# Optimization experiments

Measured on AMD Instinct MI355X. Metric: run time of the kernel, lower is better.

## Reference

```python
import jax, jax.numpy as jnp
import numpy as np

B, N, D, H = 2, 1536, 1024, 16
DH = D // H
SCALE = DH ** -0.5


def setup_inputs() -> dict:
    key = jax.random.key(0)
    ks = jax.random.split(key, 16)
    s = D ** -0.5
    x = jax.random.normal(ks[0], (B, N, D), dtype=jnp.float32)
    # causal prior: 0 on/below diagonal, -1e9 above
    causal = jnp.tril(jnp.ones((N, N), dtype=bool))
    attn_bias = jnp.where(causal, 0.0, -1e9).astype(jnp.float32)[None, None]
    mk = lambda k, shp: jax.random.normal(k, shp, dtype=jnp.float32) * s
    return {
        "x": x,
        "attn_bias": attn_bias,
        "Wq": mk(ks[1], (D, D)), "bq": jnp.zeros((D,), jnp.float32),
        "Wk": mk(ks[2], (D, D)), "bk": jnp.zeros((D,), jnp.float32),
        "Wv": mk(ks[3], (D, D)), "bv": jnp.zeros((D,), jnp.float32),
        "Wg1": mk(ks[4], (D, D)), "bg1": jnp.zeros((D,), jnp.float32),
        "Wg2": mk(ks[5], (D, 1)), "bg2": jnp.zeros((1,), jnp.float32),
        "Wo": mk(ks[6], (D, D)), "bo": jnp.zeros((D,), jnp.float32),
    }


def reference(x, attn_bias, Wq, bq, Wk, bk, Wv, bv, Wg1, bg1, Wg2, bg2, Wo, bo):
    b, n, d = x.shape
    # projections -> [B, H, N, DH]
    split = lambda t: t.reshape(b, n, H, DH).swapaxes(1, 2)
    Q = split(x @ Wq + bq)
    K = split(x @ Wk + bk)
    V = split(x @ Wv + bv)
    # scores [B, H, N, N]
    attn = jnp.einsum("bhnd,bhmd->bhnm", Q, K) * SCALE + attn_bias
    attn = jax.nn.softmax(attn, axis=-1)
    # per-(batch, head, query) entropy over key axis
    entropy = -(attn * jnp.log(attn + 1e-6)).sum(-1)  # [B, H, N]
    # gate MLP (torch nn.GELU default is exact erf)
    gate = jax.nn.sigmoid(jax.nn.gelu(x @ Wg1 + bg1, approximate=False) @ Wg2 + bg2)  # [B, N, 1]
    attn = attn * gate[:, None, :, :]  # broadcast over heads, keys
    out = jnp.einsum("bhnm,bhmd->bhnd", attn, V)
    out = out.swapaxes(1, 2).reshape(b, n, d) @ Wo + bo
    return out, entropy
```

## Files before the change

kernel.cpp:

```cpp
#include <hip/hip_runtime.h>
#include <hip/hip_bf16.h>
#include <math.h>

#define Bsz  2
#define Nseq 1536
#define Dmod 1024
#define NH   16
#define DHd  64
#define MTOT (Bsz*Nseq)
#define SCALE 0.125f
#define BK   32

typedef short  short8 __attribute__((ext_vector_type(8)));
typedef float  f32x4  __attribute__((ext_vector_type(4)));
typedef unsigned short u16x4 __attribute__((ext_vector_type(4)));
typedef unsigned short ushortT;

__device__ __forceinline__ float b2f(__hip_bfloat16 v) { return __bfloat162float(v); }
__device__ __forceinline__ unsigned short f2bf(float f) {
    union { float f; unsigned u; } a; a.f = f;
    unsigned r = a.u + 0x7fffu + ((a.u >> 16) & 1u);
    return (unsigned short)(r >> 16);
}

__device__ __forceinline__ void gl2lds16(const ushortT* g, ushortT* lds) {
    __builtin_amdgcn_global_load_lds(
        (const __attribute__((address_space(1))) unsigned int*)(g),
        (__attribute__((address_space(3))) unsigned int*)(lds),
        16, 0, 0);
}

__global__ __launch_bounds__(256)
void prep_kernel(const float* W0, const float* W1, const float* W2,
                 const float* W3, const float* W4,
                 ushortT* T0, ushortT* T1, ushortT* T2, ushortT* T3, ushortT* T4,
                 const float* __restrict__ x, ushortT* __restrict__ xb,
                 float* __restrict__ glogit)
{
    const int z = blockIdx.z;
    const int t = threadIdx.x;
    if (z == 5) {
        const int bi = blockIdx.y * 16 + blockIdx.x;
        const size_t NEl = (size_t)MTOT * Dmod;
        for (size_t i = ((size_t)bi * 256 + t) * 4; i < NEl; i += (size_t)256 * 256 * 4) {
            float4 v = *(const float4*)(x + i);
            u16x4 o = { f2bf(v.x), f2bf(v.y), f2bf(v.z), f2bf(v.w) };
            *(u16x4*)(xb + i) = o;
        }
        if (t < 12) glogit[bi * 12 + t] = 0.f;
        return;
    }
    __shared__ float tile[64][65];
    const float* W = z == 0 ? W0 : z == 1 ? W1 : z == 2 ? W2 : z == 3 ? W3 : W4;
    ushortT*     T = z == 0 ? T0 : z == 1 ? T1 : z == 2 ? T2 : z == 3 ? T3 : T4;
    const int k0 = blockIdx.x * 64, n0 = blockIdx.y * 64;
    for (int i = t; i < 1024; i += 256) {
        int r = i >> 4, c4 = (i & 15) * 4;
        float4 v = *(const float4*)&W[(size_t)(k0 + r) * 1024 + n0 + c4];
        tile[r][c4 + 0] = v.x; tile[r][c4 + 1] = v.y;
        tile[r][c4 + 2] = v.z; tile[r][c4 + 3] = v.w;
    }
    __syncthreads();
    for (int i = t; i < 1024; i += 256) {
        int rn = i >> 4, ck4 = (i & 15) * 4;
        u16x4 o = { f2bf(tile[ck4 + 0][rn]), f2bf(tile[ck4 + 1][rn]),
                    f2bf(tile[ck4 + 2][rn]), f2bf(tile[ck4 + 3][rn]) };
        *(u16x4*)&T[(size_t)(n0 + rn) * 1024 + k0 + ck4] = o;
    }
}

__device__ __forceinline__
void gemm_core(const ushortT* __restrict__ A, const ushortT* __restrict__ Bt,
               int m0, int n0, ushortT* As, ushortT* Bs, f32x4 (&acc)[4][2])
{
    const int t = threadIdx.x;
    const int l = t & 63, w = t >> 6;
    const int wm = (w >> 1) * 64, wn = (w & 1) * 32;
    const int lm = l & 15, q = l >> 4;

    const int r0 = t >> 2, c0 = (t & 3) * 8;
    const ushortT* Ag0 = A  + (size_t)(m0 + r0) * 1024 + c0;
    const ushortT* Ag1 = Ag0 + (size_t)64 * 1024;
    const ushortT* Bg0 = Bt + (size_t)(n0 + r0) * 1024 + c0;
    ushortT* La0 = As + t * 8;
    ushortT* La1 = As + 2048 + t * 8;
    ushortT* Lb0 = Bs + t * 8;

    gl2lds16(Ag0, La0);
    gl2lds16(Ag1, La1);
    gl2lds16(Bg0, Lb0);

    for (int kt = 0; kt < 1024 / BK; ++kt) {
        __syncthreads();
        if (kt + 1 < 1024 / BK) {
            int ko = (kt + 1) * BK;
            int bo = ((kt + 1) & 1) ? 4096 : 0;
            int bo2 = ((kt + 1) & 1) ? 2048 : 0;
            gl2lds16(Ag0 + ko, La0 + bo);
            gl2lds16(Ag1 + ko, La1 + bo);
            gl2lds16(Bg0 + ko, Lb0 + bo2);
        }
        const ushortT* Ab = As + ((kt & 1) ? 4096 : 0);
        const ushortT* Bb = Bs + ((kt & 1) ? 2048 : 0);
        short8 af[4], bf[2];
#pragma unroll
        for (int i = 0; i < 4; ++i)
            af[i] = *(const short8*)&Ab[(wm + i * 16 + lm) * 32 + q * 8];
#pragma unroll
        for (int j = 0; j < 2; ++j)
            bf[j] = *(const short8*)&Bb[(wn + j * 16 + lm) * 32 + q * 8];
#pragma unroll
        for (int i = 0; i < 4; ++i)
#pragma unroll
            for (int j = 0; j < 2; ++j)
                acc[i][j] = __builtin_amdgcn_mfma_f32_16x16x32_bf16(af[i], bf[j], acc[i][j], 0, 0, 0);
    }
}

__device__ __forceinline__
void gemm_core_sq(const ushortT* __restrict__ A, const ushortT* __restrict__ Bt,
                  int m0, int n0, ushortT* As, ushortT* Bs, f32x4 (&acc)[2][2])
{
    const int t = threadIdx.x;
    const int l = t & 63, w = t >> 6;
    const int wm = (w >> 1) * 32, wn = (w & 1) * 32;
    const int lm = l & 15, q = l >> 4;

    const int r0 = t >> 2, c0 = (t & 3) * 8;
    const ushortT* Ag = A  + (size_t)(m0 + r0) * 1024 + c0;
    const ushortT* Bg = Bt + (size_t)(n0 + r0) * 1024 + c0;
    ushortT* La = As + t * 8;
    ushortT* Lb = Bs + t * 8;

    gl2lds16(Ag, La);
    gl2lds16(Bg, Lb);

    for (int kt = 0; kt < 1024 / BK; ++kt) {
        __syncthreads();
        if (kt + 1 < 1024 / BK) {
            int ko = (kt + 1) * BK;
            int bo = ((kt + 1) & 1) ? 2048 : 0;
            gl2lds16(Ag + ko, La + bo);
            gl2lds16(Bg + ko, Lb + bo);
        }
        const ushortT* Ab = As + ((kt & 1) ? 2048 : 0);
        const ushortT* Bb = Bs + ((kt & 1) ? 2048 : 0);
        short8 af[2], bf[2];
#pragma unroll
        for (int i = 0; i < 2; ++i) {
            af[i] = *(const short8*)&Ab[(wm + i * 16 + lm) * 32 + q * 8];
            bf[i] = *(const short8*)&Bb[(wn + i * 16 + lm) * 32 + q * 8];
        }
#pragma unroll
        for (int i = 0; i < 2; ++i)
#pragma unroll
            for (int j = 0; j < 2; ++j)
                acc[i][j] = __builtin_amdgcn_mfma_f32_16x16x32_bf16(af[i], bf[j], acc[i][j], 0, 0, 0);
    }
}

__global__ __launch_bounds__(256)
void gemm_qkvg(const ushortT* __restrict__ xb,
               const ushortT* Wt0, const ushortT* Wt1, const ushortT* Wt2, const ushortT* Wt3,
               const float* bz0, const float* bz1, const float* bz2, const float* bz3,
               const float* __restrict__ Wg2,
               ushortT* O0, ushortT* O1, ushortT* O2, float* __restrict__ glogit)
{
    __shared__ ushortT As[2 * 128 * 32];
    __shared__ ushortT Bs[2 * 64 * 32];
    const int z = blockIdx.z;
    const ushortT* Wt  = z == 0 ? Wt0 : z == 1 ? Wt1 : z == 2 ? Wt2 : Wt3;
    const float*  bias = z == 0 ? bz0 : z == 1 ? bz1 : z == 2 ? bz2 : bz3;
    const int m0 = blockIdx.y * 128, n0 = blockIdx.x * 64;

    f32x4 acc[4][2] = {};
    gemm_core(xb, Wt, m0, n0, As, Bs, acc);

    const int t = threadIdx.x, l = t & 63, w = t >> 6;
    const int wm = (w >> 1) * 64, wn = (w & 1) * 32;
    const int lm = l & 15, q = l >> 4;

    if (z == 3) {
        float part[4][4] = {};
#pragma unroll
        for (int i = 0; i < 4; ++i)
#pragma unroll
            for (int j = 0; j < 2; ++j) {
                int n = n0 + wn + j * 16 + lm;
                float bn = bias[n];
                float w2 = Wg2[n];
#pragma unroll
                for (int r = 0; r < 4; ++r) {
                    float v = acc[i][j][r] + bn;
                    v = 0.5f * v * (1.0f + erff(v * 0.70710678118654752f));
                    part[i][r] += v * w2;
                }
            }
#pragma unroll
        for (int i = 0; i < 4; ++i)
#pragma unroll
            for (int r = 0; r < 4; ++r) {
                float p = part[i][r];
#pragma unroll
                for (int msk = 1; msk < 16; msk <<= 1) p += __shfl_xor(p, msk, 16);
                if (lm == 0)
                    atomicAdd(&glogit[m0 + wm + i * 16 + q * 4 + r], p);
            }
        return;
    }

    ushortT* O = z == 0 ? O0 : z == 1 ? O1 : O2;
#pragma unroll
    for (int i = 0; i < 4; ++i)
#pragma unroll
        for (int j = 0; j < 2; ++j) {
            int n = n0 + wn + j * 16 + lm;
            float bn = bias[n];
#pragma unroll
            for (int r = 0; r < 4; ++r) {
                int m = m0 + wm + i * 16 + q * 4 + r;
                float v = acc[i][j][r] + bn;
                if (z == 0) v *= SCALE;
                if (z == 2) {
                    int b = m / Nseq, nn = m - b * Nseq;
                    int h = n >> 6, dd = n & 63;
                    O[(size_t)((b * 16 + h) * 64 + dd) * Nseq + nn] = f2bf(v);
                } else {
                    O[(size_t)m * 1024 + n] = f2bf(v);
                }
            }
        }
}

__global__ __launch_bounds__(256)
void gemm_out(const ushortT* __restrict__ AO, const ushortT* __restrict__ WtO,
              const float* __restrict__ bias, float* __restrict__ C)
{
    __shared__ ushortT As[2 * 64 * 32];
    __shared__ ushortT Bs[2 * 64 * 32];
    const int m0 = blockIdx.y * 64, n0 = blockIdx.x * 64;

    f32x4 acc[2][2] = {};
    gemm_core_sq(AO, WtO, m0, n0, As, Bs, acc);

    const int t = threadIdx.x, l = t & 63, w = t >> 6;
    const int wm = (w >> 1) * 32, wn = (w & 1) * 32;
    const int lm = l & 15, q = l >> 4;
#pragma unroll
    for (int i = 0; i < 2; ++i)
#pragma unroll
        for (int j = 0; j < 2; ++j) {
            int n = n0 + wn + j * 16 + lm;
            float bn = bias[n];
#pragma unroll
            for (int r = 0; r < 4; ++r) {
                int m = m0 + wm + i * 16 + q * 4 + r;
                C[(size_t)m * 1024 + n] = acc[i][j][r] + bn;
            }
        }
}

__global__ __launch_bounds__(128)
void attn_mfma(const ushortT* __restrict__ Q, const ushortT* __restrict__ K,
               const ushortT* __restrict__ Vt, const float* __restrict__ glogit,
               const float* __restrict__ bg2, ushortT* __restrict__ AO,
               float* __restrict__ ent)
{
    __shared__ ushortT Ps[2][32][72];
    __shared__ float mbuf[3072];

    const int t  = threadIdx.x;
    const int w  = t >> 6, l = t & 63;
    const int ln = l & 15, q4 = l >> 4;
    const int bh = blockIdx.x, b = bh >> 4, h = bh & 15;
    const int q32 = (int)gridDim.y - 1 - (int)blockIdx.y;
    const int wq = q32 * 32;
    const int kd = wq >> 6;
    const int sbmax = ((wq >> 4) & 3) + 1;

    const ushortT* Qp = Q + (size_t)(b * Nseq + wq + ln) * Dmod + h * DHd + q4 * 8;
    short8 qf[2][2];
    qf[0][0] = *(const short8*)(Qp);
    qf[0][1] = *(const short8*)(Qp + 32);
    qf[1][0] = *(const short8*)(Qp + (size_t)16 * Dmod);
    qf[1][1] = *(const short8*)(Qp + (size_t)16 * Dmod + 32);

    float l_lane[2][4] = {}, t_lane[2][4] = {};
    f32x4 oacc[2][4] = {};

    const ushortT* Kbase = K  + (size_t)(b * Nseq) * Dmod + h * DHd + q4 * 8;
    const ushortT* Vbase = Vt + ((size_t)(b * 16 + h) * 64) * Nseq + q4 * 8;

    short8 kc[4][2];
    {
        const ushortT* Kp = Kbase + (size_t)(w * 64 + ln) * Dmod;
#pragma unroll
        for (int nb = 0; nb < 4; ++nb) {
            kc[nb][0] = *(const short8*)(Kp + (size_t)nb * 16 * Dmod);
            kc[nb][1] = *(const short8*)(Kp + (size_t)nb * 16 * Dmod + 32);
        }
    }

    for (int kt = w; kt < kd; kt += 2) {
        const int k0 = kt * 64;
        const ushortT* Vp = Vbase + (size_t)ln * Nseq + k0;
        short8 vf[4][2];
#pragma unroll
        for (int nb = 0; nb < 4; ++nb) {
            vf[nb][0] = *(const short8*)(Vp + (size_t)nb * 16 * Nseq);
            vf[nb][1] = *(const short8*)(Vp + (size_t)nb * 16 * Nseq + 32);
        }
        short8 kn[4][2];
        {
            int prow = k0 + 128; if (prow > Nseq - 64) prow = Nseq - 64;
            const ushortT* Kp = Kbase + (size_t)(prow + ln) * Dmod;
#pragma unroll
            for (int nb = 0; nb < 4; ++nb) {
                kn[nb][0] = *(const short8*)(Kp + (size_t)nb * 16 * Dmod);
                kn[nb][1] = *(const short8*)(Kp + (size_t)nb * 16 * Dmod + 32);
            }
        }
        f32x4 sacc[2][4];
#pragma unroll
        for (int g = 0; g < 2; ++g)
#pragma unroll
            for (int nb = 0; nb < 4; ++nb) {
                f32x4 a = {};
                a = __builtin_amdgcn_mfma_f32_16x16x32_bf16(qf[g][0], kc[nb][0], a, 0, 0, 0);
                a = __builtin_amdgcn_mfma_f32_16x16x32_bf16(qf[g][1], kc[nb][1], a, 0, 0, 0);
                sacc[g][nb] = a;
            }
#pragma unroll
        for (int g = 0; g < 2; ++g)
#pragma unroll
            for (int nb = 0; nb < 4; ++nb)
#pragma unroll
                for (int r = 0; r < 4; ++r) {
                    float sv = sacc[g][nb][r];
                    float ev = __expf(sv);
                    l_lane[g][r] += ev;
                    t_lane[g][r] += ev * sv;
                    Ps[w][g * 16 + q4 * 4 + r][nb * 16 + ln] = f2bf(ev);
                }
        short8 pf[2][2];
#pragma unroll
        for (int g = 0; g < 2; ++g) {
            pf[g][0] = *(const short8*)&Ps[w][g * 16 + ln][q4 * 8];
            pf[g][1] = *(const short8*)&Ps[w][g * 16 + ln][32 + q4 * 8];
        }
#pragma unroll
        for (int g = 0; g < 2; ++g)
#pragma unroll
            for (int nb = 0; nb < 4; ++nb) {
                oacc[g][nb] = __builtin_amdgcn_mfma_f32_16x16x32_bf16(pf[g][0], vf[nb][0], oacc[g][nb], 0, 0, 0);
                oacc[g][nb] = __builtin_amdgcn_mfma_f32_16x16x32_bf16(pf[g][1], vf[nb][1], oacc[g][nb], 0, 0, 0);
            }
#pragma unroll
        for (int nb = 0; nb < 4; ++nb) { kc[nb][0] = kn[nb][0]; kc[nb][1] = kn[nb][1]; }
    }

    if ((kd & 1) == w) {
        const int k0 = kd * 64;
        const ushortT* Vp = Vbase + (size_t)ln * Nseq + k0;
        short8 vf[4][2];
#pragma unroll
        for (int nb = 0; nb < 4; ++nb) {
            vf[nb][0] = *(const short8*)(Vp + (size_t)nb * 16 * Nseq);
            vf[nb][1] = *(const short8*)(Vp + (size_t)nb * 16 * Nseq + 32);
        }
        f32x4 sacc[2][4];
#pragma unroll
        for (int g = 0; g < 2; ++g)
#pragma unroll
            for (int nb = 0; nb < 4; ++nb)
                if (nb <= sbmax) {
                    f32x4 a = {};
                    a = __builtin_amdgcn_mfma_f32_16x16x32_bf16(qf[g][0], kc[nb][0], a, 0, 0, 0);
                    a = __builtin_amdgcn_mfma_f32_16x16x32_bf16(qf[g][1], kc[nb][1], a, 0, 0, 0);
                    sacc[g][nb] = a;
                }
#pragma unroll
        for (int g = 0; g < 2; ++g)
#pragma unroll
            for (int nb = 0; nb < 4; ++nb)
#pragma unroll
                for (int r = 0; r < 4; ++r) {
                    float ev = 0.f;
                    if (nb <= sbmax) {
                        int kg = k0 + nb * 16 + ln;
                        int qg = wq + g * 16 + q4 * 4 + r;
                        float sv = sacc[g][nb][r];
                        ev = (kg <= qg) ? __expf(sv) : 0.f;
                        l_lane[g][r] += ev;
                        t_lane[g][r] += ev * sv;
                    }
                    Ps[w][g * 16 + q4 * 4 + r][nb * 16 + ln] = f2bf(ev);
                }
        short8 pf[2][2];
#pragma unroll
        for (int g = 0; g < 2; ++g) {
            pf[g][0] = *(const short8*)&Ps[w][g * 16 + ln][q4 * 8];
            pf[g][1] = *(const short8*)&Ps[w][g * 16 + ln][32 + q4 * 8];
        }
#pragma unroll
        for (int g = 0; g < 2; ++g)
#pragma unroll
            for (int nb = 0; nb < 4; ++nb) {
                oacc[g][nb] = __builtin_amdgcn_mfma_f32_16x16x32_bf16(pf[g][0], vf[nb][0], oacc[g][nb], 0, 0, 0);
                oacc[g][nb] = __builtin_amdgcn_mfma_f32_16x16x32_bf16(pf[g][1], vf[nb][1], oacc[g][nb], 0, 0, 0);
            }
    }

    if (w == 1) {
#pragma unroll
        for (int g = 0; g < 2; ++g)
#pragma unroll
            for (int nb = 0; nb < 4; ++nb)
#pragma unroll
                for (int r = 0; r < 4; ++r)
                    mbuf[(((g << 2) | nb) * 4 + r) * 64 + l] = oacc[g][nb][r];
#pragma unroll
        for (int g = 0; g < 2; ++g)
#pragma unroll
            for (int r = 0; r < 4; ++r) {
                mbuf[2048 + ((g << 2) | r) * 64 + l] = l_lane[g][r];
                mbuf[2560 + ((g << 2) | r) * 64 + l] = t_lane[g][r];
            }
    }
    __syncthreads();
    if (w == 1) return;
#pragma unroll
    for (int g = 0; g < 2; ++g) {
#pragma unroll
        for (int nb = 0; nb < 4; ++nb)
#pragma unroll
            for (int r = 0; r < 4; ++r)
                oacc[g][nb][r] += mbuf[(((g << 2) | nb) * 4 + r) * 64 + l];
#pragma unroll
        for (int r = 0; r < 4; ++r) {
            l_lane[g][r] += mbuf[2048 + ((g << 2) | r) * 64 + l];
            t_lane[g][r] += mbuf[2560 + ((g << 2) | r) * 64 + l];
        }
    }

    const float bg2v = bg2[0];
#pragma unroll
    for (int g = 0; g < 2; ++g) {
        float sc[4];
#pragma unroll
        for (int r = 0; r < 4; ++r) {
            float lv = l_lane[g][r], tv = t_lane[g][r];
#pragma unroll
            for (int msk = 1; msk < 16; msk <<= 1) {
                lv += __shfl_xor(lv, msk, 16);
                tv += __shfl_xor(tv, msk, 16);
            }
            int qg = wq + g * 16 + q4 * 4 + r;
            float inv = 1.f / lv;
            if (ln == 0)
                ent[((size_t)b * NH + h) * Nseq + qg] = logf(lv) - tv * inv;
            float logit = glogit[b * Nseq + qg] + bg2v;
            sc[r] = inv / (1.f + __expf(-logit));
        }
#pragma unroll
        for (int nb = 0; nb < 4; ++nb)
#pragma unroll
            for (int r = 0; r < 4; ++r) {
                int qg = wq + g * 16 + q4 * 4 + r;
                AO[(size_t)(b * Nseq + qg) * Dmod + h * DHd + nb * 16 + ln] =
                    f2bf(oacc[g][nb][r] * sc[r]);
            }
    }
}

extern "C" void kernel_launch(void* const* d_in, const int* in_sizes, int n_in,
                              void* d_out, int out_size, void* d_ws, size_t ws_size,
                              hipStream_t stream)
{
    const float* x   = (const float*)d_in[0];
    const float* Wq  = (const float*)d_in[2];
    const float* bq  = (const float*)d_in[3];
    const float* Wk  = (const float*)d_in[4];
    const float* bk  = (const float*)d_in[5];
    const float* Wv  = (const float*)d_in[6];
    const float* bv  = (const float*)d_in[7];
    const float* Wg1 = (const float*)d_in[8];
    const float* bg1 = (const float*)d_in[9];
    const float* Wg2 = (const float*)d_in[10];
    const float* bg2 = (const float*)d_in[11];
    const float* Wo  = (const float*)d_in[12];
    const float* bo  = (const float*)d_in[13];

    const size_t NE = (size_t)MTOT * Dmod;
    ushortT* p   = (ushortT*)d_ws;
    ushortT* Qw  = p; p += NE;
    ushortT* Kw  = p; p += NE;
    ushortT* Vtw = p; p += NE;
    ushortT* AO  = p; p += NE;
    ushortT* xb  = p; p += NE;
    ushortT* WtQ = p; p += (size_t)1024 * 1024;
    ushortT* WtK = p; p += (size_t)1024 * 1024;
    ushortT* WtV = p; p += (size_t)1024 * 1024;
    ushortT* WtG = p; p += (size_t)1024 * 1024;
    ushortT* WtO = p; p += (size_t)1024 * 1024;
    float* glogit = (float*)p;

    float* out_f = (float*)d_out;
    float* ent_f = out_f + NE;

    prep_kernel<<<dim3(16, 16, 6), 256, 0, stream>>>(Wq, Wk, Wv, Wg1, Wo,
                                                     WtQ, WtK, WtV, WtG, WtO,
                                                     x, xb, glogit);
    gemm_qkvg<<<dim3(16, 24, 4), 256, 0, stream>>>(xb, WtQ, WtK, WtV, WtG,
                                                   bq, bk, bv, bg1, Wg2,
                                                   Qw, Kw, Vtw, glogit);
    attn_mfma<<<dim3(Bsz * NH, Nseq / 32), 128, 0, stream>>>(Qw, Kw, Vtw, glogit,
                                                             bg2, AO, ent_f);
    gemm_out<<<dim3(16, 48), 256, 0, stream>>>(AO, WtO, bo, out_f);
}
```

Measured before the change: 227.4 us.

## Remap block indices for XCD-aware L2 locality and merge attention query tiles

Measured after the change: 244.1 us. +7.3%, slower.

```diff
diff --git a/kernel.cpp b/kernel.cpp
--- a/kernel.cpp
+++ b/kernel.cpp
@@ -168,10 +168,16 @@
 {
     __shared__ ushortT As[2 * 128 * 32];
     __shared__ ushortT Bs[2 * 64 * 32];
-    const int z = blockIdx.z;
+
+    const int f = (int)blockIdx.x;
+    const int cx = f & 7, j = f >> 3;
+    const int z  = j / 48;
+    const int vx = (cx & 3) * 4 + (j & 3);
+    const int vy = (cx >> 2) * 12 + ((j >> 2) % 12);
+    const int m0 = vy * 128, n0 = vx * 64;
+
     const ushortT* Wt  = z == 0 ? Wt0 : z == 1 ? Wt1 : z == 2 ? Wt2 : Wt3;
     const float*  bias = z == 0 ? bz0 : z == 1 ? bz1 : z == 2 ? bz2 : bz3;
-    const int m0 = blockIdx.y * 128, n0 = blockIdx.x * 64;
 
     f32x4 acc[4][2] = {};
     gemm_core(xb, Wt, m0, n0, As, Bs, acc);
@@ -185,13 +191,13 @@
 #pragma unroll
         for (int i = 0; i < 4; ++i)
 #pragma unroll
-            for (int j = 0; j < 2; ++j) {
-                int n = n0 + wn + j * 16 + lm;
+            for (int jj = 0; jj < 2; ++jj) {
+                int n = n0 + wn + jj * 16 + lm;
                 float bn = bias[n];
                 float w2 = Wg2[n];
 #pragma unroll
                 for (int r = 0; r < 4; ++r) {
-                    float v = acc[i][j][r] + bn;
+                    float v = acc[i][jj][r] + bn;
                     v = 0.5f * v * (1.0f + erff(v * 0.70710678118654752f));
                     part[i][r] += v * w2;
                 }
@@ -213,13 +219,13 @@
 #pragma unroll
     for (int i = 0; i < 4; ++i)
 #pragma unroll
-        for (int j = 0; j < 2; ++j) {
-            int n = n0 + wn + j * 16 + lm;
+        for (int jj = 0; jj < 2; ++jj) {
+            int n = n0 + wn + jj * 16 + lm;
             float bn = bias[n];
 #pragma unroll
             for (int r = 0; r < 4; ++r) {
                 int m = m0 + wm + i * 16 + q * 4 + r;
-                float v = acc[i][j][r] + bn;
+                float v = acc[i][jj][r] + bn;
                 if (z == 0) v *= SCALE;
                 if (z == 2) {
                     int b = m / Nseq, nn = m - b * Nseq;
@@ -238,7 +244,11 @@
 {
     __shared__ ushortT As[2 * 64 * 32];
     __shared__ ushortT Bs[2 * 64 * 32];
-    const int m0 = blockIdx.y * 64, n0 = blockIdx.x * 64;
+
+    const int f = (int)blockIdx.x;
+    const int c = f & 7, j = f >> 3;
+    const int m0 = (c * 6 + (j >> 4)) * 64;
+    const int n0 = (j & 15) * 64;
 
     f32x4 acc[2][2] = {};
     gemm_core_sq(AO, WtO, m0, n0, As, Bs, acc);
@@ -249,32 +259,38 @@
 #pragma unroll
     for (int i = 0; i < 2; ++i)
 #pragma unroll
-        for (int j = 0; j < 2; ++j) {
-            int n = n0 + wn + j * 16 + lm;
+        for (int jj = 0; jj < 2; ++jj) {
+            int n = n0 + wn + jj * 16 + lm;
             float bn = bias[n];
 #pragma unroll
             for (int r = 0; r < 4; ++r) {
                 int m = m0 + wm + i * 16 + q * 4 + r;
-                C[(size_t)m * 1024 + n] = acc[i][j][r] + bn;
-            }
-        }
-}
-
-__global__ __launch_bounds__(128)
+                C[(size_t)m * 1024 + n] = acc[i][jj][r] + bn;
+            }
+        }
+}
+
+__global__ __launch_bounds__(256)
 void attn_mfma(const ushortT* __restrict__ Q, const ushortT* __restrict__ K,
                const ushortT* __restrict__ Vt, const float* __restrict__ glogit,
                const float* __restrict__ bg2, ushortT* __restrict__ AO,
                float* __restrict__ ent)
 {
-    __shared__ ushortT Ps[2][32][72];
-    __shared__ float mbuf[3072];
+    __shared__ ushortT Ps[4][32][72];
+    __shared__ float mbuf[2][3072];
 
     const int t  = threadIdx.x;
     const int w  = t >> 6, l = t & 63;
+    const int qh = w >> 1, par = w & 1;
     const int ln = l & 15, q4 = l >> 4;
-    const int bh = blockIdx.x, b = bh >> 4, h = bh & 15;
-    const int q32 = (int)gridDim.y - 1 - (int)blockIdx.y;
-    const int wq = q32 * 32;
+
+    const int f = (int)blockIdx.x;
+    const int c = f & 7, j = f >> 3;
+    const int bh = c * 4 + (j & 3);
+    const int jj = j >> 2;
+    const int q64 = (j & 1) ? (23 - jj) : jj;
+    const int b = bh >> 4, h = bh & 15;
+    const int wq = q64 * 64 + qh * 32;
     const int kd = wq >> 6;
     const int sbmax = ((wq >> 4) & 3) + 1;
 
@@ -293,7 +309,7 @@
 
     short8 kc[4][2];
     {
-        const ushortT* Kp = Kbase + (size_t)(w * 64 + ln) * Dmod;
+        const ushortT* Kp = Kbase + (size_t)(par * 64 + ln) * Dmod;
 #pragma unroll
         for (int nb = 0; nb < 4; ++nb) {
             kc[nb][0] = *(const short8*)(Kp + (size_t)nb * 16 * Dmod);
@@ -301,7 +317,7 @@
         }
     }
 
-    for (int kt = w; kt < kd; kt += 2) {
+    for (int kt = par; kt < kd; kt += 2) {
         const int k0 = kt * 64;
         const ushortT* Vp = Vbase + (size_t)ln * Nseq + k0;
         short8 vf[4][2];
@@ -359,7 +375,7 @@
         for (int nb = 0; nb < 4; ++nb) { kc[nb][0] = kn[nb][0]; kc[nb][1] = kn[nb][1]; }
     }
 
-    if ((kd & 1) == w) {
+    if ((kd & 1) == par) {
         const int k0 = kd * 64;
         const ushortT* Vp = Vbase + (size_t)ln * Nseq + k0;
         short8 vf[4][2];
@@ -411,35 +427,35 @@
             }
     }
 
-    if (w == 1) {
+    if (par == 1) {
 #pragma unroll
         for (int g = 0; g < 2; ++g)
 #pragma unroll
             for (int nb = 0; nb < 4; ++nb)
 #pragma unroll
                 for (int r = 0; r < 4; ++r)
-                    mbuf[(((g << 2) | nb) * 4 + r) * 64 + l] = oacc[g][nb][r];
+                    mbuf[qh][(((g << 2) | nb) * 4 + r) * 64 + l] = oacc[g][nb][r];
 #pragma unroll
         for (int g = 0; g < 2; ++g)
 #pragma unroll
             for (int r = 0; r < 4; ++r) {
-                mbuf[2048 + ((g << 2) | r) * 64 + l] = l_lane[g][r];
-                mbuf[2560 + ((g << 2) | r) * 64 + l] = t_lane[g][r];
+                mbuf[qh][2048 + ((g << 2) | r) * 64 + l] = l_lane[g][r];
+                mbuf[qh][2560 + ((g << 2) | r) * 64 + l] = t_lane[g][r];
             }
     }
     __syncthreads();
-    if (w == 1) return;
+    if (par == 1) return;
 #pragma unroll
     for (int g = 0; g < 2; ++g) {
 #pragma unroll
         for (int nb = 0; nb < 4; ++nb)
 #pragma unroll
             for (int r = 0; r < 4; ++r)
-                oacc[g][nb][r] += mbuf[(((g << 2) | nb) * 4 + r) * 64 + l];
+                oacc[g][nb][r] += mbuf[qh][(((g << 2) | nb) * 4 + r) * 64 + l];
 #pragma unroll
         for (int r = 0; r < 4; ++r) {
-            l_lane[g][r] += mbuf[2048 + ((g << 2) | r) * 64 + l];
-            t_lane[g][r] += mbuf[2560 + ((g << 2) | r) * 64 + l];
+            l_lane[g][r] += mbuf[qh][2048 + ((g << 2) | r) * 64 + l];
+            t_lane[g][r] += mbuf[qh][2560 + ((g << 2) | r) * 64 + l];
         }
     }
 
@@ -511,10 +527,10 @@
     prep_kernel<<<dim3(16, 16, 6), 256, 0, stream>>>(Wq, Wk, Wv, Wg1, Wo,
                                                      WtQ, WtK, WtV, WtG, WtO,
                                                      x, xb, glogit);
-    gemm_qkvg<<<dim3(16, 24, 4), 256, 0, stream>>>(xb, WtQ, WtK, WtV, WtG,
-                                                   bq, bk, bv, bg1, Wg2,
-                                                   Qw, Kw, Vtw, glogit);
-    attn_mfma<<<dim3(Bsz * NH, Nseq / 32), 128, 0, stream>>>(Qw, Kw, Vtw, glogit,
-                                                             bg2, AO, ent_f);
-    gemm_out<<<dim3(16, 48), 256, 0, stream>>>(AO, WtO, bo, out_f);
-}
+    gemm_qkvg<<<dim3(1536), 256, 0, stream>>>(xb, WtQ, WtK, WtV, WtG,
+                                              bq, bk, bv, bg1, Wg2,
+                                              Qw, Kw, Vtw, glogit);
+    attn_mfma<<<dim3(768), 256, 0, stream>>>(Qw, Kw, Vtw, glogit,
+                                             bg2, AO, ent_f);
+    gemm_out<<<dim3(768), 256, 0, stream>>>(AO, WtO, bo, out_f);
+}
```
